# Kernel tuning notes

Measured on AMD Instinct MI355X. Metric: run time of the kernel, lower is better.

The kernel has to match this reference:

```python
import jax, jax.numpy as jnp
import numpy as np

NUM_NODES = 50000

def setup_inputs() -> dict:
    key = jax.random.key(0)
    k1, k2 = jax.random.split(key)
    x = jax.random.normal(k1, (NUM_NODES, 64), dtype=jnp.float32)
    edge_index = jax.random.randint(k2, (2, 800000), 0, NUM_NODES, dtype=jnp.int64)
    return {"x": x, "edge_index": edge_index}

def reference(x, edge_index):
    # gather source-node features along edges, scatter-mean into target nodes
    row, col = edge_index[0], edge_index[1]
    num_nodes = x.shape[0]
    gathered = x[row]  # [E, D]
    summed = jax.ops.segment_sum(gathered, col, num_segments=num_nodes)  # [N, D]
    count = jax.ops.segment_sum(jnp.ones_like(col, dtype=x.dtype), col, num_segments=num_nodes)  # [N]
    # mean with divide-by-zero guard (matches torch_geometric scatter reduce='mean')
    out = summed / jnp.maximum(count, 1.0)[:, None]
    return out
```

## Files before the change

kernel.cpp:

```cpp
#include <hip/hip_runtime.h>

#define N_NODES 50000
#define DIM 64
#define NPB 32
#define NB 1563
#define NCHUNK 128
#define CAPB 1024
#define CAP 1024

typedef unsigned short ushort_t;

__device__ __forceinline__ ushort_t f32_to_bf16(float f) {
    unsigned u = __float_as_uint(f);
    u += 0x7FFFu + ((u >> 16) & 1u);
    return (ushort_t)(u >> 16);
}

__device__ __forceinline__ void acc_pair(float& a0, float& a1, unsigned u) {
    a0 += __uint_as_float(u << 16);
    a1 += __uint_as_float(u & 0xFFFF0000u);
}

__global__ void init_cursor_kernel(int* __restrict__ cursor) {
    int t = blockIdx.x * blockDim.x + threadIdx.x;
    if (t <= NB) cursor[t] = t * CAPB;
}

__global__ void binning_kernel(const float* __restrict__ xf,
                               ushort_t* __restrict__ xh,
                               const int* __restrict__ row,
                               const int* __restrict__ col,
                               int* __restrict__ cursor,
                               unsigned* __restrict__ packed,
                               int E, int chunk, int n4) {
    __shared__ int h[NB];
    __shared__ int lcur[NB];
    int c = blockIdx.x;
    int tid = threadIdx.x;
    for (int i = c * blockDim.x + tid; i < n4; i += gridDim.x * blockDim.x) {
        float4 v = *reinterpret_cast<const float4*>(xf + (size_t)i * 4);
        ushort4 hh;
        hh.x = f32_to_bf16(v.x);
        hh.y = f32_to_bf16(v.y);
        hh.z = f32_to_bf16(v.z);
        hh.w = f32_to_bf16(v.w);
        *reinterpret_cast<ushort4*>(xh + (size_t)i * 4) = hh;
    }
    for (int b = tid; b < NB; b += blockDim.x) h[b] = 0;
    __syncthreads();
    int beg = c * chunk, end = min(beg + chunk, E);
    int nfull = (end - beg) >> 2;
    for (int g = tid; g < nfull; g += blockDim.x) {
        int4 c4 = *reinterpret_cast<const int4*>(col + beg + g * 4);
        atomicAdd(&h[c4.x >> 5], 1);
        atomicAdd(&h[c4.y >> 5], 1);
        atomicAdd(&h[c4.z >> 5], 1);
        atomicAdd(&h[c4.w >> 5], 1);
    }
    for (int e = beg + nfull * 4 + tid; e < end; e += blockDim.x)
        atomicAdd(&h[col[e] >> 5], 1);
    __syncthreads();
    for (int b = tid; b < NB; b += blockDim.x) {
        int v = h[b];
        lcur[b] = (v > 0) ? atomicAdd(&cursor[b], v) : 0;
    }
    __syncthreads();
    for (int g = tid; g < nfull; g += blockDim.x) {
        int e = beg + g * 4;
        int4 d4 = *reinterpret_cast<const int4*>(col + e);
        int4 s4 = *reinterpret_cast<const int4*>(row + e);
        int p0 = atomicAdd(&lcur[d4.x >> 5], 1);
        packed[p0] = (unsigned)s4.x | ((unsigned)(d4.x & 31) << 16);
        int p1 = atomicAdd(&lcur[d4.y >> 5], 1);
        packed[p1] = (unsigned)s4.y | ((unsigned)(d4.y & 31) << 16);
        int p2 = atomicAdd(&lcur[d4.z >> 5], 1);
        packed[p2] = (unsigned)s4.z | ((unsigned)(d4.z & 31) << 16);
        int p3 = atomicAdd(&lcur[d4.w >> 5], 1);
        packed[p3] = (unsigned)s4.w | ((unsigned)(d4.w & 31) << 16);
    }
    for (int e = beg + nfull * 4 + tid; e < end; e += blockDim.x) {
        int d = col[e];
        int p = atomicAdd(&lcur[d >> 5], 1);
        packed[p] = (unsigned)row[e] | ((unsigned)(d & 31) << 16);
    }
}

template <bool BF16>
__global__ __launch_bounds__(512)
void aggregate_bucket_kernel(const float* __restrict__ xf,
                             const ushort_t* __restrict__ xh,
                             const unsigned* __restrict__ packed,
                             const int* __restrict__ cursor,
                             float* __restrict__ out) {
    __shared__ unsigned short srcs[CAP];
    __shared__ int hist[NPB];
    __shared__ int segoff[NPB];
    __shared__ int lcur[NPB];

    int b = blockIdx.x;
    int tid = threadIdx.x;
    int lane = tid & 63;
    int wv = tid >> 6;
    int g8 = lane >> 3;
    int o = lane & 7;
    int seg_beg = b * CAPB;
    int m = cursor[b] - seg_beg;
    int node_base = b * NPB;
    int nnodes = min(NPB, N_NODES - node_base);

    if (tid < NPB) hist[tid] = 0;
    __syncthreads();

    unsigned v0 = 0, v1 = 0;
    int i0 = tid, i1 = tid + 512;
    if (i0 < m) { v0 = packed[seg_beg + i0]; atomicAdd(&hist[v0 >> 16], 1); }
    if (i1 < m) { v1 = packed[seg_beg + i1]; atomicAdd(&hist[v1 >> 16], 1); }
    __syncthreads();

    if (tid < NPB) {
        int v = hist[tid];
        int incl = v;
        #pragma unroll
        for (int ofs = 1; ofs < 32; ofs <<= 1) {
            int t = __shfl_up(incl, ofs);
            if (lane >= ofs) incl += t;
        }
        segoff[tid] = incl - v;
        lcur[tid] = incl - v;
    }
    __syncthreads();

    if (i0 < m) { int p = atomicAdd(&lcur[v0 >> 16], 1); srcs[p] = (unsigned short)(v0 & 0xFFFF); }
    if (i1 < m) { int p = atomicAdd(&lcur[v1 >> 16], 1); srcs[p] = (unsigned short)(v1 & 0xFFFF); }
    __syncthreads();

    float acc[4][8];
    #pragma unroll
    for (int r = 0; r < 4; ++r)
        #pragma unroll
        for (int k = 0; k < 8; ++k) acc[r][k] = 0.0f;

    #pragma unroll
    for (int r = 0; r < 4; ++r) {
        int ln = wv * 4 + r;
        int st = segoff[ln];
        int len = hist[ln];
        int j = 0;
        for (; j + 16 <= len; j += 16) {
            int s0 = srcs[st + j + g8];
            int s1 = srcs[st + j + 8 + g8];
            if (BF16) {
                uint4 a0 = *reinterpret_cast<const uint4*>(xh + (size_t)s0 * DIM + o * 8);
                uint4 a1 = *reinterpret_cast<const uint4*>(xh + (size_t)s1 * DIM + o * 8);
                acc_pair(acc[r][0], acc[r][1], a0.x);
                acc_pair(acc[r][2], acc[r][3], a0.y);
                acc_pair(acc[r][4], acc[r][5], a0.z);
                acc_pair(acc[r][6], acc[r][7], a0.w);
                acc_pair(acc[r][0], acc[r][1], a1.x);
                acc_pair(acc[r][2], acc[r][3], a1.y);
                acc_pair(acc[r][4], acc[r][5], a1.z);
                acc_pair(acc[r][6], acc[r][7], a1.w);
            } else {
                float4 u0 = *reinterpret_cast<const float4*>(xf + (size_t)s0 * DIM + o * 8);
                float4 u1 = *reinterpret_cast<const float4*>(xf + (size_t)s0 * DIM + o * 8 + 4);
                float4 u2 = *reinterpret_cast<const float4*>(xf + (size_t)s1 * DIM + o * 8);
                float4 u3 = *reinterpret_cast<const float4*>(xf + (size_t)s1 * DIM + o * 8 + 4);
                acc[r][0] += u0.x + u2.x; acc[r][1] += u0.y + u2.y;
                acc[r][2] += u0.z + u2.z; acc[r][3] += u0.w + u2.w;
                acc[r][4] += u1.x + u3.x; acc[r][5] += u1.y + u3.y;
                acc[r][6] += u1.z + u3.z; acc[r][7] += u1.w + u3.w;
            }
        }
        for (; j < len; j += 8) {
            if (j + g8 < len) {
                int s = srcs[st + j + g8];
                if (BF16) {
                    uint4 a0 = *reinterpret_cast<const uint4*>(xh + (size_t)s * DIM + o * 8);
                    acc_pair(acc[r][0], acc[r][1], a0.x);
                    acc_pair(acc[r][2], acc[r][3], a0.y);
                    acc_pair(acc[r][4], acc[r][5], a0.z);
                    acc_pair(acc[r][6], acc[r][7], a0.w);
                } else {
                    float4 u0 = *reinterpret_cast<const float4*>(xf + (size_t)s * DIM + o * 8);
                    float4 u1 = *reinterpret_cast<const float4*>(xf + (size_t)s * DIM + o * 8 + 4);
                    acc[r][0] += u0.x; acc[r][1] += u0.y;
                    acc[r][2] += u0.z; acc[r][3] += u0.w;
                    acc[r][4] += u1.x; acc[r][5] += u1.y;
                    acc[r][6] += u1.z; acc[r][7] += u1.w;
                }
            }
        }
    }
    __syncthreads();
    #pragma unroll
    for (int r = 0; r < 4; ++r) {
        int ln = wv * 4 + r;
        #pragma unroll
        for (int k = 0; k < 8; ++k) {
            acc[r][k] += __shfl_xor(acc[r][k], 8);
            acc[r][k] += __shfl_xor(acc[r][k], 16);
            acc[r][k] += __shfl_xor(acc[r][k], 32);
        }
        if (g8 == 0 && ln < nnodes) {
            int c = hist[ln];
            float inv = (c > 0) ? 1.0f / (float)c : 0.0f;
            float* op = out + (size_t)(node_base + ln) * DIM + o * 8;
            #pragma unroll
            for (int k = 0; k < 8; ++k)
                __builtin_nontemporal_store(acc[r][k] * inv, op + k);
        }
    }
}

extern "C" void kernel_launch(void* const* d_in, const int* in_sizes, int n_in,
                              void* d_out, int out_size, void* d_ws, size_t ws_size,
                              hipStream_t stream) {
    const float* x = (const float*)d_in[0];
    const int* edge_index = (const int*)d_in[1];
    int E = in_sizes[1] / 2;
    const int* row = edge_index;
    const int* col = edge_index + E;
    float* out = (float*)d_out;

    int chunk = (((E + NCHUNK - 1) / NCHUNK) + 3) & ~3;
    int n4 = N_NODES * DIM / 4;

    int* cursor      = (int*)d_ws;
    unsigned* packed = (unsigned*)(cursor + 1568);
    ushort_t* xh     = (ushort_t*)(packed + (size_t)NB * CAPB);
    size_t need_bf16 = (size_t)((char*)(xh + (size_t)N_NODES * DIM) - (char*)d_ws);
    bool use_bf16 = (ws_size >= need_bf16);

    init_cursor_kernel<<<7, 256, 0, stream>>>(cursor);
    binning_kernel<<<NCHUNK, 1024, 0, stream>>>(x, xh, row, col, cursor, packed,
                                                E, chunk, use_bf16 ? n4 : 0);
    if (use_bf16)
        aggregate_bucket_kernel<true><<<NB, 512, 0, stream>>>(x, xh, packed, cursor, out);
    else
        aggregate_bucket_kernel<false><<<NB, 512, 0, stream>>>(x, xh, packed, cursor, out);
}
```

Measured before the change: 52.89 us.

## Split bf16 feature table into two half-width planes and aggregate in two passes

The bf16 copy of node features is stored as two separate planes, one holding feature columns 0-31 and one holding columns 32-63. Aggregation runs in two passes, one per plane, with 16 edges per wave (4 lanes per row) instead of 8. The aim is to halve the gather working set per pass so it fits better in cache and to get more edges in flight per load. In exchange, the srcs indices and the segment loop are walked twice, there is an extra shuffle stage, and the output is written in two half-rows. The conversion kernel is also widened to 8 floats per thread.

```diff
diff --git a/kernel.cpp b/kernel.cpp
--- a/kernel.cpp
+++ b/kernel.cpp
@@ -10,10 +10,10 @@
 
 typedef unsigned short ushort_t;
 
-__device__ __forceinline__ ushort_t f32_to_bf16(float f) {
+__device__ __forceinline__ unsigned f32_to_bf16u(float f) {
     unsigned u = __float_as_uint(f);
     u += 0x7FFFu + ((u >> 16) & 1u);
-    return (ushort_t)(u >> 16);
+    return u >> 16;
 }
 
 __device__ __forceinline__ void acc_pair(float& a0, float& a1, unsigned u) {
@@ -27,24 +27,30 @@
 }
 
 __global__ void binning_kernel(const float* __restrict__ xf,
-                               ushort_t* __restrict__ xh,
+                               ushort_t* __restrict__ xh_lo,
+                               ushort_t* __restrict__ xh_hi,
                                const int* __restrict__ row,
                                const int* __restrict__ col,
                                int* __restrict__ cursor,
                                unsigned* __restrict__ packed,
-                               int E, int chunk, int n4) {
+                               int E, int chunk, int n8) {
     __shared__ int h[NB];
     __shared__ int lcur[NB];
     int c = blockIdx.x;
     int tid = threadIdx.x;
-    for (int i = c * blockDim.x + tid; i < n4; i += gridDim.x * blockDim.x) {
-        float4 v = *reinterpret_cast<const float4*>(xf + (size_t)i * 4);
-        ushort4 hh;
-        hh.x = f32_to_bf16(v.x);
-        hh.y = f32_to_bf16(v.y);
-        hh.z = f32_to_bf16(v.z);
-        hh.w = f32_to_bf16(v.w);
-        *reinterpret_cast<ushort4*>(xh + (size_t)i * 4) = hh;
+    for (int g = c * blockDim.x + tid; g < n8; g += gridDim.x * blockDim.x) {
+        const float* xp = xf + (size_t)g * 8;
+        float4 v0 = *reinterpret_cast<const float4*>(xp);
+        float4 v1 = *reinterpret_cast<const float4*>(xp + 4);
+        uint4 h4;
+        h4.x = f32_to_bf16u(v0.x) | (f32_to_bf16u(v0.y) << 16);
+        h4.y = f32_to_bf16u(v0.z) | (f32_to_bf16u(v0.w) << 16);
+        h4.z = f32_to_bf16u(v1.x) | (f32_to_bf16u(v1.y) << 16);
+        h4.w = f32_to_bf16u(v1.z) | (f32_to_bf16u(v1.w) << 16);
+        int rown = g >> 3;
+        int oct = g & 7;
+        ushort_t* plane = (oct < 4) ? xh_lo : xh_hi;
+        *reinterpret_cast<uint4*>(plane + (size_t)rown * 32 + (oct & 3) * 8) = h4;
     }
     for (int b = tid; b < NB; b += blockDim.x) h[b] = 0;
     __syncthreads();
@@ -88,7 +94,8 @@
 template <bool BF16>
 __global__ __launch_bounds__(512)
 void aggregate_bucket_kernel(const float* __restrict__ xf,
-                             const ushort_t* __restrict__ xh,
+                             const ushort_t* __restrict__ xh_lo,
+                             const ushort_t* __restrict__ xh_hi,
                              const unsigned* __restrict__ packed,
                              const int* __restrict__ cursor,
                              float* __restrict__ out) {
@@ -101,8 +108,8 @@
     int tid = threadIdx.x;
     int lane = tid & 63;
     int wv = tid >> 6;
-    int g8 = lane >> 3;
-    int o = lane & 7;
+    int g16 = lane >> 2;
+    int o4 = lane & 3;
     int seg_beg = b * CAPB;
     int m = cursor[b] - seg_beg;
     int node_base = b * NPB;
@@ -134,80 +141,76 @@
     if (i1 < m) { int p = atomicAdd(&lcur[v1 >> 16], 1); srcs[p] = (unsigned short)(v1 & 0xFFFF); }
     __syncthreads();
 
-    float acc[4][8];
     #pragma unroll
-    for (int r = 0; r < 4; ++r)
-        #pragma unroll
-        for (int k = 0; k < 8; ++k) acc[r][k] = 0.0f;
-
-    #pragma unroll
-    for (int r = 0; r < 4; ++r) {
-        int ln = wv * 4 + r;
-        int st = segoff[ln];
-        int len = hist[ln];
-        int j = 0;
-        for (; j + 16 <= len; j += 16) {
-            int s0 = srcs[st + j + g8];
-            int s1 = srcs[st + j + 8 + g8];
-            if (BF16) {
-                uint4 a0 = *reinterpret_cast<const uint4*>(xh + (size_t)s0 * DIM + o * 8);
-                uint4 a1 = *reinterpret_cast<const uint4*>(xh + (size_t)s1 * DIM + o * 8);
-                acc_pair(acc[r][0], acc[r][1], a0.x);
-                acc_pair(acc[r][2], acc[r][3], a0.y);
-                acc_pair(acc[r][4], acc[r][5], a0.z);
-                acc_pair(acc[r][6], acc[r][7], a0.w);
-                acc_pair(acc[r][0], acc[r][1], a1.x);
-                acc_pair(acc[r][2], acc[r][3], a1.y);
-                acc_pair(acc[r][4], acc[r][5], a1.z);
-                acc_pair(acc[r][6], acc[r][7], a1.w);
-            } else {
-                float4 u0 = *reinterpret_cast<const float4*>(xf + (size_t)s0 * DIM + o * 8);
-                float4 u1 = *reinterpret_cast<const float4*>(xf + (size_t)s0 * DIM + o * 8 + 4);
-                float4 u2 = *reinterpret_cast<const float4*>(xf + (size_t)s1 * DIM + o * 8);
-                float4 u3 = *reinterpret_cast<const float4*>(xf + (size_t)s1 * DIM + o * 8 + 4);
-                acc[r][0] += u0.x + u2.x; acc[r][1] += u0.y + u2.y;
-                acc[r][2] += u0.z + u2.z; acc[r][3] += u0.w + u2.w;
-                acc[r][4] += u1.x + u3.x; acc[r][5] += u1.y + u3.y;
-                acc[r][6] += u1.z + u3.z; acc[r][7] += u1.w + u3.w;
-            }
-        }
-        for (; j < len; j += 8) {
-            if (j + g8 < len) {
-                int s = srcs[st + j + g8];
+    for (int ph = 0; ph < 2; ++ph) {
+        const ushort_t* plane = ph ? xh_hi : xh_lo;
+        float acc[4][8];
+        #pragma unroll
+        for (int r = 0; r < 4; ++r)
+            #pragma unroll
+            for (int k = 0; k < 8; ++k) acc[r][k] = 0.0f;
+
+        #pragma unroll
+        for (int r = 0; r < 4; ++r) {
+            int ln = wv * 4 + r;
+            int st = segoff[ln];
+            int len = hist[ln];
+            int j = 0;
+            for (; j + 16 <= len; j += 16) {
+                int s = srcs[st + j + g16];
                 if (BF16) {
-                    uint4 a0 = *reinterpret_cast<const uint4*>(xh + (size_t)s * DIM + o * 8);
-                    acc_pair(acc[r][0], acc[r][1], a0.x);
-                    acc_pair(acc[r][2], acc[r][3], a0.y);
-                    acc_pair(acc[r][4], acc[r][5], a0.z);
-                    acc_pair(acc[r][6], acc[r][7], a0.w);
+                    uint4 a = *reinterpret_cast<const uint4*>(plane + (size_t)s * 32 + o4 * 8);
+                    acc_pair(acc[r][0], acc[r][1], a.x);
+                    acc_pair(acc[r][2], acc[r][3], a.y);
+                    acc_pair(acc[r][4], acc[r][5], a.z);
+                    acc_pair(acc[r][6], acc[r][7], a.w);
                 } else {
-                    float4 u0 = *reinterpret_cast<const float4*>(xf + (size_t)s * DIM + o * 8);
-                    float4 u1 = *reinterpret_cast<const float4*>(xf + (size_t)s * DIM + o * 8 + 4);
+                    const float* rp = xf + (size_t)s * DIM + ph * 32 + o4 * 8;
+                    float4 u0 = *reinterpret_cast<const float4*>(rp);
+                    float4 u1 = *reinterpret_cast<const float4*>(rp + 4);
                     acc[r][0] += u0.x; acc[r][1] += u0.y;
                     acc[r][2] += u0.z; acc[r][3] += u0.w;
                     acc[r][4] += u1.x; acc[r][5] += u1.y;
                     acc[r][6] += u1.z; acc[r][7] += u1.w;
                 }
             }
+            if (j + g16 < len) {
+                int s = srcs[st + j + g16];
+                if (BF16) {
+                    uint4 a = *reinterpret_cast<const uint4*>(plane + (size_t)s * 32 + o4 * 8);
+                    acc_pair(acc[r][0], acc[r][1], a.x);
+                    acc_pair(acc[r][2], acc[r][3], a.y);
+                    acc_pair(acc[r][4], acc[r][5], a.z);
+                    acc_pair(acc[r][6], acc[r][7], a.w);
+                } else {
+                    const float* rp = xf + (size_t)s * DIM + ph * 32 + o4 * 8;
+                    float4 u0 = *reinterpret_cast<const float4*>(rp);
+                    float4 u1 = *reinterpret_cast<const float4*>(rp + 4);
+                    acc[r][0] += u0.x; acc[r][1] += u0.y;
+                    acc[r][2] += u0.z; acc[r][3] += u0.w;
+                    acc[r][4] += u1.x; acc[r][5] += u1.y;
+                    acc[r][6] += u1.z; acc[r][7] += u1.w;
+                }
+            }
         }
-    }
-    __syncthreads();
-    #pragma unroll
-    for (int r = 0; r < 4; ++r) {
-        int ln = wv * 4 + r;
-        #pragma unroll
-        for (int k = 0; k < 8; ++k) {
-            acc[r][k] += __shfl_xor(acc[r][k], 8);
-            acc[r][k] += __shfl_xor(acc[r][k], 16);
-            acc[r][k] += __shfl_xor(acc[r][k], 32);
-        }
-        if (g8 == 0 && ln < nnodes) {
-            int c = hist[ln];
-            float inv = (c > 0) ? 1.0f / (float)c : 0.0f;
-            float* op = out + (size_t)(node_base + ln) * DIM + o * 8;
+        #pragma unroll
+        for (int r = 0; r < 4; ++r) {
+            int ln = wv * 4 + r;
             #pragma unroll
-            for (int k = 0; k < 8; ++k)
-                __builtin_nontemporal_store(acc[r][k] * inv, op + k);
+            for (int k = 0; k < 8; ++k) {
+                acc[r][k] += __shfl_xor(acc[r][k], 4);
+                acc[r][k] += __shfl_xor(acc[r][k], 8);
+                acc[r][k] += __shfl_xor(acc[r][k], 16);
+                acc[r][k] += __shfl_xor(acc[r][k], 32);
+            }
+            if (g16 == 0 && ln < nnodes) {
+                int c = hist[ln];
+                float inv = (c > 0) ? 1.0f / (float)c : 0.0f;
+                float* op = out + (size_t)(node_base + ln) * DIM + ph * 32 + o4 * 8;
+                #pragma unroll
+                for (int k = 0; k < 8; ++k)
+                    __builtin_nontemporal_store(acc[r][k] * inv, op + k);
+            }
         }
     }
 }
@@ -223,19 +226,20 @@
     float* out = (float*)d_out;
 
     int chunk = (((E + NCHUNK - 1) / NCHUNK) + 3) & ~3;
-    int n4 = N_NODES * DIM / 4;
+    int n8 = N_NODES * DIM / 8;
 
     int* cursor      = (int*)d_ws;
     unsigned* packed = (unsigned*)(cursor + 1568);
-    ushort_t* xh     = (ushort_t*)(packed + (size_t)NB * CAPB);
-    size_t need_bf16 = (size_t)((char*)(xh + (size_t)N_NODES * DIM) - (char*)d_ws);
+    ushort_t* xh_lo  = (ushort_t*)(packed + (size_t)NB * CAPB);
+    ushort_t* xh_hi  = xh_lo + (size_t)N_NODES * 32;
+    size_t need_bf16 = (size_t)((char*)(xh_hi + (size_t)N_NODES * 32) - (char*)d_ws);
     bool use_bf16 = (ws_size >= need_bf16);
 
     init_cursor_kernel<<<7, 256, 0, stream>>>(cursor);
-    binning_kernel<<<NCHUNK, 1024, 0, stream>>>(x, xh, row, col, cursor, packed,
-                                                E, chunk, use_bf16 ? n4 : 0);
+    binning_kernel<<<NCHUNK, 1024, 0, stream>>>(x, xh_lo, xh_hi, row, col, cursor,
+                                                packed, E, chunk, use_bf16 ? n8 : 0);
     if (use_bf16)
-        aggregate_bucket_kernel<true><<<NB, 512, 0, stream>>>(x, xh, packed, cursor, out);
+        aggregate_bucket_kernel<true><<<NB, 512, 0, stream>>>(x, xh_lo, xh_hi, packed, cursor, out);
     else
-        aggregate_bucket_kernel<false><<<NB, 512, 0, stream>>>(x, xh, packed, cursor, out);
-}
+        aggregate_bucket_kernel<false><<<NB, 512, 0, stream>>>(x, xh_lo, xh_hi, packed, cursor, out);
+}
```

After: 71.60 us. +35.4%, slower.
